# Kernel tuning notes

Hardware: AMD Instinct MI355X
Metric: run time of the kernel (lower is better)

The kernel has to match this reference:

```python
import jax, jax.numpy as jnp
import numpy as np
from jax import lax

B, SQ, SK, D, K = 4, 2048, 2048, 1024, 3


def setup_inputs() -> dict:
    key = jax.random.key(0)
    ks = jax.random.split(key, 16)
    s = 0.02
    return {
        "query_hidden": jax.random.normal(ks[0], (B, SQ, D), jnp.float32),
        "memory_hidden": jax.random.normal(ks[1], (B, SK, D), jnp.float32),
        "attention_mask": jax.random.randint(ks[2], (SQ, SK), 0, 2).astype(bool),
        # Linear projections (torch: y = x @ W.T + b)
        "q_w": jax.random.normal(ks[3], (D, D), jnp.float32) * s,
        "q_b": jnp.zeros((D,), jnp.float32),
        "k_w": jax.random.normal(ks[4], (D, D), jnp.float32) * s,
        "k_b": jnp.zeros((D,), jnp.float32),
        "v_w": jax.random.normal(ks[5], (D, D), jnp.float32) * s,
        "v_b": jnp.zeros((D,), jnp.float32),
        "o_w": jax.random.normal(ks[6], (D, D), jnp.float32) * s,
        "o_b": jnp.zeros((D,), jnp.float32),
        # ConvTransform1D: depthwise conv kernels [D,1,K], bias [D], scalar gate
        "q_kernel": jax.random.normal(ks[7], (D, 1, K), jnp.float32) * s,
        "q_cbias": jnp.zeros((D,), jnp.float32),
        "q_gate": jnp.zeros((), jnp.float32),
        "k_kernel": jax.random.normal(ks[8], (D, 1, K), jnp.float32) * s,
        "k_cbias": jnp.zeros((D,), jnp.float32),
        "k_gate": jnp.zeros((), jnp.float32),
        "v_kernel": jax.random.normal(ks[9], (D, 1, K), jnp.float32) * s,
        "v_cbias": jnp.zeros((D,), jnp.float32),
        "v_gate": jnp.zeros((), jnp.float32),
    }


def _conv_transform(x, kernel, cbias, gate):
    """Gated depthwise 1D conv along seq: x + tanh(gate) * dwconv(x). x: [B,S,D]."""
    xc = jnp.transpose(x, (0, 2, 1))  # [B,D,S]
    y = lax.conv_general_dilated(
        xc, kernel, window_strides=(1,), padding="SAME",
        dimension_numbers=("NCH", "OIH", "NCH"), feature_group_count=x.shape[-1])
    y = y + cbias[None, :, None]
    return x + jnp.tanh(gate) * jnp.transpose(y, (0, 2, 1))


def reference(query_hidden, memory_hidden, attention_mask,
              q_w, q_b, k_w, k_b, v_w, v_b, o_w, o_b,
              q_kernel, q_cbias, q_gate,
              k_kernel, k_cbias, k_gate,
              v_kernel, v_cbias, v_gate):
    d_model = query_hidden.shape[-1]
    q = _conv_transform(query_hidden @ q_w.T + q_b, q_kernel, q_cbias, q_gate)
    k = _conv_transform(memory_hidden @ k_w.T + k_b, k_kernel, k_cbias, k_gate)
    v = _conv_transform(memory_hidden @ v_w.T + v_b, v_kernel, v_cbias, v_gate)
    # [B,Sq,Sk]
    logits = jnp.einsum("bqd,bkd->bqk", q, k) / jnp.sqrt(jnp.float32(d_model))
    mask = attention_mask[None, :, :]  # broadcast like torch unsqueeze(0)
    logits = jnp.where(mask, logits, jnp.finfo(logits.dtype).min)
    attn = jax.nn.softmax(logits, axis=-1)
    out = jnp.einsum("bqk,bkd->bqd", attn, v) @ o_w.T + o_b
    return out
```

## Files before the change

### kernel.cpp

```cpp
#include <hip/hip_runtime.h>
#include <cstdint>
#include <cstddef>


#define GLOBAL_AS __attribute__((address_space(1)))
#define LDS_AS    __attribute__((address_space(3)))

typedef _Float16 h8 __attribute__((ext_vector_type(8)));
typedef float    f4_t __attribute__((ext_vector_type(4)));
typedef unsigned short us8 __attribute__((ext_vector_type(8)));

__device__ __forceinline__ float bf2f(unsigned short u) {
    union { unsigned int i; float f; } x; x.i = ((unsigned int)u) << 16; return x.f;
}
__device__ __forceinline__ float rd(const void* p, long i, int isBf) {
    return isBf ? bf2f(((const unsigned short*)p)[i]) : ((const float*)p)[i];
}

struct Probe16 { const unsigned short* p[16]; int n[16]; };

__global__ void k_probes(Probe16 a, const unsigned int* __restrict__ mask,
                         int* __restrict__ flags) {
    if (blockIdx.x < 16) {
        __shared__ int cnt;
        if (threadIdx.x == 0) cnt = 0;
        __syncthreads();
        const unsigned short* s = a.p[blockIdx.x];
        const int n = a.n[blockIdx.x];
        int bad = 0;
        for (int i = threadIdx.x; i < n; i += 256) {
            int e = (s[i] >> 7) & 0xFF;
            if (e >= 0x8F || (e > 0 && e <= 0x60)) bad++;
        }
        atomicAdd(&cnt, bad);
        __syncthreads();
        if (threadIdx.x == 0) flags[blockIdx.x] = (cnt * 4 > n) ? 0 : 1;
    } else {
        __shared__ int vi32, vf32, vbf, vf16;
        if (threadIdx.x == 0) { vi32 = vf32 = vbf = vf16 = 0; }
        __syncthreads();
        int bi32 = 0, bf32 = 0, bbf = 0, bf16c = 0;
        for (int i = threadIdx.x; i < 4096; i += 256) {
            unsigned int w = mask[i];
            if (!(w == 0u || w == 1u)) bi32++;
            if (!(w == 0u || w == 0x3F800000u)) bf32++;
            unsigned int h0 = w & 0xFFFFu, h1 = w >> 16;
            if (!((h0 == 0u || h0 == 0x3F80u) && (h1 == 0u || h1 == 0x3F80u))) bbf++;
            if (!((h0 == 0u || h0 == 0x3C00u) && (h1 == 0u || h1 == 0x3C00u))) bf16c++;
        }
        if (bi32) atomicAdd(&vi32, 1);
        if (bf32) atomicAdd(&vf32, 1);
        if (bbf)  atomicAdd(&vbf, 1);
        if (bf16c) atomicAdd(&vf16, 1);
        __syncthreads();
        if (threadIdx.x == 0) {
            int w;
            if (vi32 == 0) w = 4;
            else if (vf32 == 0) w = 4;
            else if (vbf == 0) w = 2;
            else if (vf16 == 0) w = 2;
            else w = 1;
            flags[16] = w;
        }
    }
}

__device__ __forceinline__ h8 cvt8(const void* src, size_t off8, int isBf) {
    h8 d;
    if (isBf) {
        us8 s = *(const us8*)((const unsigned short*)src + off8 * 8);
#pragma unroll
        for (int u = 0; u < 8; ++u) d[u] = (_Float16)bf2f(s[u]);
    } else {
        const float* f = (const float*)src + off8 * 8;
        f4_t a = *(const f4_t*)f;
        f4_t b = *(const f4_t*)(f + 4);
#pragma unroll
        for (int u = 0; u < 4; ++u) { d[u] = (_Float16)a[u]; d[4 + u] = (_Float16)b[u]; }
    }
    return d;
}

struct Ptr4 { const void* p[4]; };

__global__ void k_prep(const void* __restrict__ qh, const void* __restrict__ mh,
                       _Float16* __restrict__ h16dst,
                       Ptr4 wsrc, _Float16* __restrict__ w16dst,
                       const int* __restrict__ flags) {
    const int bid = blockIdx.x, tid = threadIdx.x;
    if (bid < 8192) {
        int i = bid * 256 + tid;
        int seg = i >> 20, off = i & 1048575;
        h8 d = cvt8(seg ? mh : qh, off, flags[seg]);
        *(h8*)(h16dst + (size_t)i * 8) = d;
    } else {
        int i = (bid - 8192) * 256 + tid;
        int seg = i >> 17, off = i & 131071;
        h8 d = cvt8(wsrc.p[seg], off, flags[2 + seg]);
        *(h8*)(w16dst + (size_t)i * 8) = d;
    }
}

struct ConvSrc { const void* kern[3]; const void* cb[3]; const void* gate[3]; };
__global__ void k_conv_params(ConvSrc p, const int* __restrict__ flags,
                              _Float16* __restrict__ out, float* __restrict__ tg, int D) {
#pragma unroll
    for (int t = 0; t < 3; ++t) {
        const int kIs = flags[6 + t], cIs = flags[13 + t];
        for (int d = threadIdx.x; d < D; d += 256) {
#pragma unroll
            for (int j = 0; j < 3; ++j)
                out[t * 3 * D + j * D + d] = (_Float16)rd(p.kern[t], (long)d * 3 + j, kIs);
            out[9 * D + t * D + d] = (_Float16)rd(p.cb[t], d, cIs);
        }
    }
    if (threadIdx.x < 3) {
        const void* g = p.gate[threadIdx.x];
        float gv = rd(g, 0, ((const unsigned int*)g)[0] == 0u ? 1 : 0);
        tg[threadIdx.x] = tanhf(gv);
    }
}

template <int MODE, int MTILE>
__global__ __launch_bounds__(256, 4) void k_gemm_nt(
    const _Float16* __restrict__ A, const _Float16* __restrict__ Bm,
    void* __restrict__ Cout,
    const void* __restrict__ bias, const int* __restrict__ biasFlag,
    const void* __restrict__ bias2, const int* __restrict__ biasFlag2,
    int N, int K, long sA, long sB, long sC,
    int NT, int BZ) {

    constexpr int NI = (MTILE == 128) ? 4 : 2;
    constexpr int NCA = MTILE / 32;
    __shared__ __align__(16) _Float16 As[MTILE * 64];
    __shared__ __align__(16) _Float16 Bs[128 * 64];

    const long id = blockIdx.x;
    const int xcd = (int)(id & 7);
    const long local = id >> 3;
    const int col = (int)(local % NT);
    const long g = (local / NT) * 8 + xcd;
    const int bz = (int)(g % BZ);
    const int brow = (int)(g / BZ);

    const int tid  = threadIdx.x;
    const int wave = tid >> 6, lane = tid & 63;
    const int wm = (wave >> 1) * (MTILE / 2), wn = (wave & 1) * 64;
    const int lr = lane & 15, lq = lane >> 4;

    const _Float16* Ab = A + (long)bz * sA + (size_t)brow * MTILE * K;
    const _Float16* Bb = Bm + (long)bz * sB + (size_t)col * 128 * K;

    f4_t acc[NI][4] = {};

    const _Float16* gA[NCA];
    _Float16* lA[NCA];
#pragma unroll
    for (int j = 0; j < NCA; ++j) {
        int c = tid + j * 256;
        int r = c >> 3, s = ((c & 7) - r) & 7;
        gA[j] = Ab + (size_t)r * K + s * 8;
        lA[j] = As + c * 8;
    }
    const _Float16* gB[4];
    _Float16* lB[4];
#pragma unroll
    for (int j = 0; j < 4; ++j) {
        int c = tid + j * 256;
        int r = c >> 3, s = ((c & 7) - r) & 7;
        gB[j] = Bb + (size_t)r * K + s * 8;
        lB[j] = Bs + c * 8;
    }

    for (int kb = 0; kb < K; kb += 64) {
#pragma unroll
        for (int j = 0; j < NCA; ++j)
            __builtin_amdgcn_global_load_lds((void GLOBAL_AS*)(gA[j] + kb), (void LDS_AS*)lA[j], 16, 0, 0);
#pragma unroll
        for (int j = 0; j < 4; ++j)
            __builtin_amdgcn_global_load_lds((void GLOBAL_AS*)(gB[j] + kb), (void LDS_AS*)lB[j], 16, 0, 0);
        __syncthreads();

#pragma unroll
        for (int t = 0; t < 2; ++t) {
            const int fs = ((t * 4 + lq + lr) & 7) * 8;
            h8 af[NI], bfr[4];
#pragma unroll
            for (int i = 0; i < NI; ++i) af[i]  = *(const h8*)&As[(wm + i * 16 + lr) * 64 + fs];
#pragma unroll
            for (int j = 0; j < 4; ++j) bfr[j] = *(const h8*)&Bs[(wn + j * 16 + lr) * 64 + fs];
#pragma unroll
            for (int i = 0; i < NI; ++i)
#pragma unroll
                for (int j = 0; j < 4; ++j)
                    acc[i][j] = __builtin_amdgcn_mfma_f32_16x16x32_f16(af[i], bfr[j], acc[i][j], 0, 0, 0);
        }
        __syncthreads();
    }

    const long row0 = (long)brow * MTILE + wm + lq * 4;
    const long col0 = (long)col * 128 + wn + lr;

    float bv[4];
    if constexpr (MODE != 0) {
        const void* bp = bias; const int* bfp = biasFlag; long boff = 0;
        if (bias2 != nullptr && col * 128 >= (N >> 1)) {
            bp = bias2; bfp = biasFlag2; boff = (long)(N >> 1);
        }
        const int bIs = *bfp;
#pragma unroll
        for (int j = 0; j < 4; ++j) bv[j] = rd(bp, col0 + j * 16 - boff, bIs);
    } else {
#pragma unroll
        for (int j = 0; j < 4; ++j) bv[j] = 0.0f;
    }
    if constexpr (MODE == 2) {
        float* C = (float*)Cout + (long)bz * sC;
#pragma unroll
        for (int i = 0; i < NI; ++i)
#pragma unroll
            for (int j = 0; j < 4; ++j)
#pragma unroll
                for (int r = 0; r < 4; ++r)
                    C[(row0 + i * 16 + r) * (long)N + col0 + j * 16] = acc[i][j][r] + bv[j];
    } else {
        _Float16* C = (_Float16*)Cout + (long)bz * sC;
#pragma unroll
        for (int i = 0; i < NI; ++i)
#pragma unroll
            for (int j = 0; j < 4; ++j)
#pragma unroll
                for (int r = 0; r < 4; ++r) {
                    float v = acc[i][j][r] + bv[j];
                    v = fminf(fmaxf(v, -65000.0f), 65000.0f);
                    C[(row0 + i * 16 + r) * (long)N + col0 + j * 16] = (_Float16)v;
                }
    }
}

template <int MODE>
__global__ __launch_bounds__(512, 2) void k_gemm16(
    const _Float16* __restrict__ A, const _Float16* __restrict__ Bm,
    void* __restrict__ Cout,
    const void* __restrict__ bias, const int* __restrict__ biasFlag,
    const void* __restrict__ bias2, const int* __restrict__ biasFlag2,
    int N, int K, long sA, long sB, long sC,
    float scale, const void* __restrict__ mraw, const int* __restrict__ mwf,
    int NT, int BZ) {

    __shared__ __align__(16) _Float16 AS[2][2][8192];
    __shared__ __align__(16) _Float16 BS[2][2][8192];

    const long id = blockIdx.x;
    const int xcd = (int)(id & 7);
    const long local = id >> 3;
    const int col = (int)(local % NT);
    const long g = (local / NT) * 8 + xcd;
    const int bz = (int)(g % BZ);
    const int brow = (int)(g / BZ);

    const int tid  = threadIdx.x;
    const int wave = tid >> 6, lane = tid & 63;
    const int wr = wave >> 2, wc = wave & 3;
    const int lr = lane & 15, lq = lane >> 4;

    const _Float16* Ab = A + (long)bz * sA + (size_t)brow * 256 * K;
    const _Float16* Bb = Bm + (long)bz * sB + (size_t)col * 256 * K;

    f4_t acc[8][4] = {};

    const _Float16* gAsrc[2][2];
    const _Float16* gBsrc[2][2];
    int lOff[2];
#pragma unroll
    for (int j = 0; j < 2; ++j) {
        int c = tid + j * 512;
        int rho = c >> 3, s = ((c & 7) - rho) & 7;
        lOff[j] = c * 8;
#pragma unroll
        for (int gg = 0; gg < 2; ++gg) {
            int ra = gg * 64 + (rho & 63) + (rho >> 6) * 128;
            gAsrc[gg][j] = Ab + (size_t)ra * K + s * 8;
            int rb = gg * 32 + (rho & 31) + (rho >> 5) * 64;
            gBsrc[gg][j] = Bb + (size_t)rb * K + s * 8;
        }
    }

#define STAGE_A(buf, gg, kb)                                                              \
    do {                                                                                  \
        __builtin_amdgcn_global_load_lds((void GLOBAL_AS*)(gAsrc[gg][0] + (kb)),          \
                                         (void LDS_AS*)&AS[buf][gg][lOff[0]], 16, 0, 0);  \
        __builtin_amdgcn_global_load_lds((void GLOBAL_AS*)(gAsrc[gg][1] + (kb)),          \
                                         (void LDS_AS*)&AS[buf][gg][lOff[1]], 16, 0, 0);  \
    } while (0)
#define STAGE_B(buf, gg, kb)                                                              \
    do {                                                                                  \
        __builtin_amdgcn_global_load_lds((void GLOBAL_AS*)(gBsrc[gg][0] + (kb)),          \
                                         (void LDS_AS*)&BS[buf][gg][lOff[0]], 16, 0, 0);  \
        __builtin_amdgcn_global_load_lds((void GLOBAL_AS*)(gBsrc[gg][1] + (kb)),          \
                                         (void LDS_AS*)&BS[buf][gg][lOff[1]], 16, 0, 0);  \
    } while (0)

    const int nkt = K >> 6;

    STAGE_A(0, 0, 0);
    STAGE_B(0, 0, 0);
    STAGE_B(0, 1, 0);
    STAGE_A(0, 1, 0);
    asm volatile("s_waitcnt vmcnt(4)" ::: "memory");
    __builtin_amdgcn_s_barrier();

    int cur = 0;
    for (int t = 0; t < nkt; ++t) {
        const bool pf = (t + 1) < nkt;
        const long kb = (long)(t + 1) << 6;
        const int nx = cur ^ 1;
        h8 a0[4][2], a1[4][2], b0[2][2], b1[2][2];

#pragma unroll
        for (int ks = 0; ks < 2; ++ks) {
#pragma unroll
            for (int m = 0; m < 4; ++m) {
                int rho = wr * 64 + m * 16 + lr;
                a0[m][ks] = *(const h8*)&AS[cur][0][rho * 64 + ((ks * 4 + lq + rho) & 7) * 8];
            }
#pragma unroll
            for (int n = 0; n < 2; ++n) {
                int rho = wc * 32 + n * 16 + lr;
                b0[n][ks] = *(const h8*)&BS[cur][0][rho * 64 + ((ks * 4 + lq + rho) & 7) * 8];
            }
        }
        if (pf) STAGE_A(nx, 0, kb);
        __builtin_amdgcn_s_barrier();
        __builtin_amdgcn_s_setprio(1);
#pragma unroll
        for (int ks = 0; ks < 2; ++ks)
#pragma unroll
            for (int m = 0; m < 4; ++m)
#pragma unroll
                for (int n = 0; n < 2; ++n)
                    acc[m][n] = __builtin_amdgcn_mfma_f32_16x16x32_f16(
                        a0[m][ks], b0[n][ks], acc[m][n], 0, 0, 0);
        __builtin_amdgcn_s_setprio(0);
        if (pf) asm volatile("s_waitcnt vmcnt(4)" ::: "memory");
        else    asm volatile("s_waitcnt vmcnt(2)" ::: "memory");
        __builtin_amdgcn_s_barrier();

#pragma unroll
        for (int ks = 0; ks < 2; ++ks)
#pragma unroll
            for (int n = 0; n < 2; ++n) {
                int rho = wc * 32 + n * 16 + lr;
                b1[n][ks] = *(const h8*)&BS[cur][1][rho * 64 + ((ks * 4 + lq + rho) & 7) * 8];
            }
        if (pf) STAGE_B(nx, 0, kb);
        __builtin_amdgcn_s_barrier();
        __builtin_amdgcn_s_setprio(1);
#pragma unroll
        for (int ks = 0; ks < 2; ++ks)
#pragma unroll
            for (int m = 0; m < 4; ++m)
#pragma unroll
                for (int n = 0; n < 2; ++n)
                    acc[m][2 + n] = __builtin_amdgcn_mfma_f32_16x16x32_f16(
                        a0[m][ks], b1[n][ks], acc[m][2 + n], 0, 0, 0);
        __builtin_amdgcn_s_setprio(0);
        if (pf) asm volatile("s_waitcnt vmcnt(4)" ::: "memory");
        else    asm volatile("s_waitcnt vmcnt(0)" ::: "memory");
        __builtin_amdgcn_s_barrier();

#pragma unroll
        for (int ks = 0; ks < 2; ++ks)
#pragma unroll
            for (int m = 0; m < 4; ++m) {
                int rho = wr * 64 + m * 16 + lr;
                a1[m][ks] = *(const h8*)&AS[cur][1][rho * 64 + ((ks * 4 + lq + rho) & 7) * 8];
            }
        if (pf) STAGE_B(nx, 1, kb);
        __builtin_amdgcn_s_barrier();
        __builtin_amdgcn_s_setprio(1);
#pragma unroll
        for (int ks = 0; ks < 2; ++ks)
#pragma unroll
            for (int m = 0; m < 4; ++m)
#pragma unroll
                for (int n = 0; n < 2; ++n)
                    acc[4 + m][2 + n] = __builtin_amdgcn_mfma_f32_16x16x32_f16(
                        a1[m][ks], b1[n][ks], acc[4 + m][2 + n], 0, 0, 0);
        __builtin_amdgcn_s_setprio(0);
        __builtin_amdgcn_s_barrier();

#pragma unroll
        for (int ks = 0; ks < 2; ++ks)
#pragma unroll
            for (int n = 0; n < 2; ++n) {
                int rho = wc * 32 + n * 16 + lr;
                b0[n][ks] = *(const h8*)&BS[cur][0][rho * 64 + ((ks * 4 + lq + rho) & 7) * 8];
            }
        if (pf) STAGE_A(nx, 1, kb);
        __builtin_amdgcn_s_barrier();
        __builtin_amdgcn_s_setprio(1);
#pragma unroll
        for (int ks = 0; ks < 2; ++ks)
#pragma unroll
            for (int m = 0; m < 4; ++m)
#pragma unroll
                for (int n = 0; n < 2; ++n)
                    acc[4 + m][n] = __builtin_amdgcn_mfma_f32_16x16x32_f16(
                        a1[m][ks], b0[n][ks], acc[4 + m][n], 0, 0, 0);
        __builtin_amdgcn_s_setprio(0);
        if (pf) asm volatile("s_waitcnt vmcnt(4)" ::: "memory");
        __builtin_amdgcn_s_barrier();
        cur = nx;
    }
#undef STAGE_A
#undef STAGE_B

    const long row0 = (long)brow * 256 + wr * 128 + lq * 4;
    const long col0 = (long)col * 256 + wc * 64 + lr;

    if constexpr (MODE == 3) {
        const int mw = *mwf;
        _Float16* C = (_Float16*)Cout + (long)bz * sC;
#pragma unroll
        for (int i = 0; i < 8; ++i)
#pragma unroll
            for (int j = 0; j < 4; ++j)
#pragma unroll
                for (int r = 0; r < 4; ++r) {
                    long row = row0 + i * 16 + r;
                    long ccol = col0 + j * 16;
                    long mi = row * (long)N + ccol;
                    bool keep;
                    if (mw == 4)      keep = ((const unsigned int*)mraw)[mi] != 0u;
                    else if (mw == 2) keep = ((const unsigned short*)mraw)[mi] != 0;
                    else              keep = ((const unsigned char*)mraw)[mi] != 0;
                    float v = acc[i][j][r] * scale;
                    v = fminf(fmaxf(v, -60000.0f), 60000.0f);
                    C[row * (long)N + ccol] = (_Float16)(keep ? v : -60000.0f);
                }
    } else {
        float bv[4];
        {
            const void* bp = bias; const int* bfp = biasFlag; long boff = 0;
            if (bias2 != nullptr && col * 256 >= (N >> 1)) {
                bp = bias2; bfp = biasFlag2; boff = (long)(N >> 1);
            }
            const int bIs = *bfp;
#pragma unroll
            for (int j = 0; j < 4; ++j) bv[j] = rd(bp, col0 + j * 16 - boff, bIs);
        }
        _Float16* C = (_Float16*)Cout + (long)bz * sC;
#pragma unroll
        for (int i = 0; i < 8; ++i)
#pragma unroll
            for (int j = 0; j < 4; ++j)
#pragma unroll
                for (int r = 0; r < 4; ++r) {
                    float v = acc[i][j][r] + bv[j];
                    v = fminf(fmaxf(v, -65000.0f), 65000.0f);
                    C[(row0 + i * 16 + r) * (long)N + col0 + j * 16] = (_Float16)v;
                }
    }
}

struct ConvP {
    const _Float16* x; int xs; _Float16* y;
    const _Float16* kp; const _Float16* cb; const float* tg;
};
__global__ void k_convs(ConvP p0, ConvP p1,
                        const _Float16* __restrict__ xv, int xvs,
                        _Float16* __restrict__ vt,
                        const _Float16* __restrict__ kpv,
                        const _Float16* __restrict__ cbv,
                        const float* __restrict__ tgv,
                        int S, int SK, int D) {
    __shared__ _Float16 T[64][65];
    const int bid = blockIdx.x, tid = threadIdx.x;
    h8 zero;
#pragma unroll
    for (int u = 0; u < 8; ++u) zero[u] = (_Float16)0.0f;

    if (bid < 8192) {
        const ConvP& p = (bid >= 4096) ? p1 : p0;
        int l = bid & 4095;
        int b = l >> 10, sp = l & 1023;
        int s = sp * 2 + (tid >> 7);
        int d0 = (tid & 127) * 8;
        const size_t xb = ((size_t)b * S + s) * p.xs + d0;
        const size_t yb = ((size_t)b * S + s) * D + d0;
        h8 xc = *(const h8*)(p.x + xb);
        h8 xp = (s > 0)     ? *(const h8*)(p.x + xb - p.xs) : zero;
        h8 xn = (s < S - 1) ? *(const h8*)(p.x + xb + p.xs) : zero;
        h8 k0 = *(const h8*)(p.kp + 0 * D + d0);
        h8 k1 = *(const h8*)(p.kp + 1 * D + d0);
        h8 k2 = *(const h8*)(p.kp + 2 * D + d0);
        h8 cb = *(const h8*)(p.cb + d0);
        float tg = *p.tg;
        h8 o;
#pragma unroll
        for (int u = 0; u < 8; ++u) {
            float cv = (float)xp[u] * (float)k0[u] + (float)xc[u] * (float)k1[u] +
                       (float)xn[u] * (float)k2[u] + (float)cb[u];
            float v = (float)xc[u] + tg * cv;
            o[u] = (_Float16)fminf(fmaxf(v, -65000.0f), 65000.0f);
        }
        *(h8*)(p.y + yb) = o;
    } else {
        int l = bid - 8192;
        int bx = l & 31, by = (l >> 5) & 15, b = l >> 9;
        int s0 = bx * 64, d0 = by * 64;
        float tg = *tgv;
#pragma unroll
        for (int it = 0; it < 2; ++it) {
            int idx = it * 256 + tid;
            int r = idx >> 3, c = (idx & 7) * 8;
            int s = s0 + r;
            const size_t xb = ((size_t)b * SK + s) * xvs + d0 + c;
            h8 xc = *(const h8*)(xv + xb);
            h8 xp = (s > 0)      ? *(const h8*)(xv + xb - xvs) : zero;
            h8 xn = (s < SK - 1) ? *(const h8*)(xv + xb + xvs) : zero;
            h8 k0 = *(const h8*)(kpv + 0 * D + d0 + c);
            h8 k1 = *(const h8*)(kpv + 1 * D + d0 + c);
            h8 k2 = *(const h8*)(kpv + 2 * D + d0 + c);
            h8 cb = *(const h8*)(cbv + d0 + c);
#pragma unroll
            for (int u = 0; u < 8; ++u) {
                float cv = (float)xp[u] * (float)k0[u] + (float)xc[u] * (float)k1[u] +
                           (float)xn[u] * (float)k2[u] + (float)cb[u];
                float v = (float)xc[u] + tg * cv;
                T[r][c + u] = (_Float16)fminf(fmaxf(v, -65000.0f), 65000.0f);
            }
        }
        __syncthreads();
#pragma unroll
        for (int it = 0; it < 2; ++it) {
            int idx = it * 256 + tid;
            int dr = idx >> 3, c = (idx & 7) * 8;
            h8 o;
#pragma unroll
            for (int u = 0; u < 8; ++u) o[u] = T[c + u][dr];
            *(h8*)(vt + ((size_t)b * D + d0 + dr) * SK + s0 + c) = o;
        }
    }
}

__global__ __launch_bounds__(256) void k_softmax(const _Float16* __restrict__ sc,
                                                 _Float16* __restrict__ pr, int SK) {
    const long row = blockIdx.x;
    const int tid = threadIdx.x, lane = tid & 63, wave = tid >> 6;
    h8 v = *(const h8*)(sc + row * (long)SK + tid * 8);
    float f[8]; float mx = -3.0e38f;
#pragma unroll
    for (int u = 0; u < 8; ++u) { f[u] = (float)v[u]; mx = fmaxf(mx, f[u]); }
#pragma unroll
    for (int o = 32; o > 0; o >>= 1) mx = fmaxf(mx, __shfl_xor(mx, o, 64));
    __shared__ float red[8];
    if (lane == 0) red[wave] = mx;
    __syncthreads();
    mx = fmaxf(fmaxf(red[0], red[1]), fmaxf(red[2], red[3]));
    float sum = 0.0f;
#pragma unroll
    for (int u = 0; u < 8; ++u) { f[u] = __expf(f[u] - mx); sum += f[u]; }
#pragma unroll
    for (int o = 32; o > 0; o >>= 1) sum += __shfl_xor(sum, o, 64);
    if (lane == 0) red[4 + wave] = sum;
    __syncthreads();
    sum = red[4] + red[5] + red[6] + red[7];
    float inv = 1.0f / sum;
    h8 o8;
#pragma unroll
    for (int u = 0; u < 8; ++u) o8[u] = (_Float16)(f[u] * inv);
    *(h8*)(pr + row * (long)SK + tid * 8) = o8;
}

extern "C" void kernel_launch(void* const* d_in, const int* in_sizes, int n_in,
                              void* d_out, int out_size, void* d_ws, size_t ws_size,
                              hipStream_t stream) {
    const int Bn = 4, SQ = 2048, SK = 2048, D = 1024;
    const size_t nQ = (size_t)Bn * SQ * D;

    const void* qh = d_in[0];
    const void* mh = d_in[1];
    const void* mask = d_in[2];
    const void* q_w = d_in[3];
    const void* q_b = d_in[4];
    const void* k_w = d_in[5];
    const void* k_b = d_in[6];
    const void* v_w = d_in[7];
    const void* v_b = d_in[8];
    const void* o_w = d_in[9];
    const void* o_b = d_in[10];
    const void* q_kern = d_in[11];
    const void* q_cb   = d_in[12];
    const void* q_g    = d_in[13];
    const void* k_kern = d_in[14];
    const void* k_cb   = d_in[15];
    const void* k_g    = d_in[16];
    const void* v_kern = d_in[17];
    const void* v_cb   = d_in[18];
    const void* v_g    = d_in[19];

    char* ws = (char*)d_ws;
    _Float16* scores   = (_Float16*)(ws + 0);
    _Float16* attn_out = (_Float16*)(ws + 0);
    _Float16* w16      = (_Float16*)(ws + 33554432);
    _Float16* par16    = (_Float16*)(ws + 37748736);
    float*    tgf      = (float*)(ws + 37748736 + 12 * 1024 * 2);
    _Float16* lin      = (_Float16*)(ws + 41943040);
    _Float16* lin_q    = lin;
    _Float16* lin_kv   = lin + nQ;
    _Float16* probs    = lin;
    _Float16* conv     = (_Float16*)(ws + 92274688);
    _Float16* qh16     = conv;
    _Float16* mh16     = conv + nQ;
    _Float16* vt       = (_Float16*)(ws + 125829120);
    int*      flags    = (int*)(ws + 142606336);

    Probe16 pa;
    const void* pp[16] = {qh, mh, q_w, k_w, v_w, o_w, q_kern, k_kern, v_kern,
                          q_b, k_b, v_b, o_b, q_cb, k_cb, v_cb};
    const int   pn[16] = {2048, 2048, 2048, 2048, 2048, 2048, 3072, 3072, 3072,
                          1024, 1024, 1024, 1024, 1024, 1024, 1024};
    for (int i = 0; i < 16; ++i) { pa.p[i] = (const unsigned short*)pp[i]; pa.n[i] = pn[i]; }
    k_probes<<<17, 256, 0, stream>>>(pa, (const unsigned int*)mask, flags);

    Ptr4 wp; wp.p[0] = q_w; wp.p[1] = k_w; wp.p[2] = v_w; wp.p[3] = o_w;
    k_prep<<<10240, 256, 0, stream>>>(qh, mh, qh16, wp, w16, flags);

    k_gemm_nt<1, 64><<<dim3(1024), 256, 0, stream>>>(
        qh16, w16, lin_q, q_b, flags + 9, nullptr, nullptr,
        D, D, 0, 0, 0, 8, 1);
    k_gemm16<1><<<dim3(256), 512, 0, stream>>>(
        mh16, w16 + (size_t)D * D, lin_kv, k_b, flags + 10, v_b, flags + 11,
        2 * D, D, 0, 0, 0, 1.0f, nullptr, nullptr, 8, 1);

    ConvSrc cs;
    cs.kern[0] = q_kern; cs.kern[1] = k_kern; cs.kern[2] = v_kern;
    cs.cb[0] = q_cb; cs.cb[1] = k_cb; cs.cb[2] = v_cb;
    cs.gate[0] = q_g; cs.gate[1] = k_g; cs.gate[2] = v_g;
    k_conv_params<<<1, 256, 0, stream>>>(cs, flags, par16, tgf, D);

    ConvP cq{lin_q, D, conv + 0 * nQ, par16 + 0 * 3 * D, par16 + 9 * D + 0 * D, tgf + 0};
    ConvP ck{lin_kv, 2 * D, conv + 1 * nQ, par16 + 1 * 3 * D, par16 + 9 * D + 1 * D, tgf + 1};
    k_convs<<<dim3(10240), 256, 0, stream>>>(
        cq, ck, lin_kv + D, 2 * D, vt, par16 + 2 * 3 * D, par16 + 9 * D + 2 * D, tgf + 2,
        SQ, SK, D);

    k_gemm16<3><<<dim3(256), 512, 0, stream>>>(
        conv + 0 * nQ, conv + 1 * nQ, scores, nullptr, nullptr, nullptr, nullptr,
        SK, D, (long)SQ * D, (long)SK * D, (long)SQ * SK, 0.03125f, mask, flags + 16, 8, 4);

    k_softmax<<<Bn * SQ, 256, 0, stream>>>(scores, probs, SK);

    k_gemm_nt<0, 64><<<dim3(1024), 256, 0, stream>>>(
        probs, vt, attn_out, nullptr, nullptr, nullptr, nullptr,
        D, SK, (long)SQ * SK, (long)D * SK, (long)SQ * D, 8, 4);

    k_gemm_nt<2, 64><<<dim3(1024), 256, 0, stream>>>(
        attn_out, w16 + 3 * (size_t)D * D, d_out, o_b, flags + 12, nullptr, nullptr,
        D, D, 0, 0, 0, 8, 1);

    (void)in_sizes; (void)n_in; (void)out_size; (void)ws_size;
}
```

Baseline: 444.9 us.

## Move attention mask application from QK GEMM epilogue into softmax; fold conv params into prep

The mask lookup moves out of the QK^T GEMM epilogue and into the softmax kernel. The GEMM epilogue no longer does scattered per-element mask loads, and softmax reads the mask row with vector loads alongside the scores. The separate single-block conv-parameter kernel is merged into k_prep as one extra block, which saves a launch. The par16/tgf workspace region is relocated, and the extra block performs the small parameter conversion serially.

```diff
diff --git a/kernel.cpp b/kernel.cpp
--- a/kernel.cpp
+++ b/kernel.cpp
@@ -82,10 +82,13 @@
 }
 
 struct Ptr4 { const void* p[4]; };
+struct ConvSrc { const void* kern[3]; const void* cb[3]; const void* gate[3]; };
 
 __global__ void k_prep(const void* __restrict__ qh, const void* __restrict__ mh,
                        _Float16* __restrict__ h16dst,
                        Ptr4 wsrc, _Float16* __restrict__ w16dst,
+                       ConvSrc cs, _Float16* __restrict__ par16,
+                       float* __restrict__ tgf,
                        const int* __restrict__ flags) {
     const int bid = blockIdx.x, tid = threadIdx.x;
     if (bid < 8192) {
@@ -93,31 +96,28 @@
         int seg = i >> 20, off = i & 1048575;
         h8 d = cvt8(seg ? mh : qh, off, flags[seg]);
         *(h8*)(h16dst + (size_t)i * 8) = d;
-    } else {
+    } else if (bid < 10240) {
         int i = (bid - 8192) * 256 + tid;
         int seg = i >> 17, off = i & 131071;
         h8 d = cvt8(wsrc.p[seg], off, flags[2 + seg]);
         *(h8*)(w16dst + (size_t)i * 8) = d;
-    }
-}
-
-struct ConvSrc { const void* kern[3]; const void* cb[3]; const void* gate[3]; };
-__global__ void k_conv_params(ConvSrc p, const int* __restrict__ flags,
-                              _Float16* __restrict__ out, float* __restrict__ tg, int D) {
-#pragma unroll
-    for (int t = 0; t < 3; ++t) {
-        const int kIs = flags[6 + t], cIs = flags[13 + t];
-        for (int d = threadIdx.x; d < D; d += 256) {
-#pragma unroll
-            for (int j = 0; j < 3; ++j)
-                out[t * 3 * D + j * D + d] = (_Float16)rd(p.kern[t], (long)d * 3 + j, kIs);
-            out[9 * D + t * D + d] = (_Float16)rd(p.cb[t], d, cIs);
-        }
-    }
-    if (threadIdx.x < 3) {
-        const void* g = p.gate[threadIdx.x];
-        float gv = rd(g, 0, ((const unsigned int*)g)[0] == 0u ? 1 : 0);
-        tg[threadIdx.x] = tanhf(gv);
+    } else {
+        const int D = 1024;
+#pragma unroll
+        for (int t = 0; t < 3; ++t) {
+            const int kIs = flags[6 + t], cIs = flags[13 + t];
+            for (int d = tid; d < D; d += 256) {
+#pragma unroll
+                for (int j = 0; j < 3; ++j)
+                    par16[t * 3 * D + j * D + d] = (_Float16)rd(cs.kern[t], (long)d * 3 + j, kIs);
+                par16[9 * D + t * D + d] = (_Float16)rd(cs.cb[t], d, cIs);
+            }
+        }
+        if (tid < 3) {
+            const void* g = cs.gate[tid];
+            float gv = rd(g, 0, ((const unsigned int*)g)[0] == 0u ? 1 : 0);
+            tgf[tid] = tanhf(gv);
+        }
     }
 }
 
@@ -245,8 +245,7 @@
     const void* __restrict__ bias, const int* __restrict__ biasFlag,
     const void* __restrict__ bias2, const int* __restrict__ biasFlag2,
     int N, int K, long sA, long sB, long sC,
-    float scale, const void* __restrict__ mraw, const int* __restrict__ mwf,
-    int NT, int BZ) {
+    float scale, int NT, int BZ) {
 
     __shared__ __align__(16) _Float16 AS[2][2][8192];
     __shared__ __align__(16) _Float16 BS[2][2][8192];
@@ -420,7 +419,6 @@
     const long col0 = (long)col * 256 + wc * 64 + lr;
 
     if constexpr (MODE == 3) {
-        const int mw = *mwf;
         _Float16* C = (_Float16*)Cout + (long)bz * sC;
 #pragma unroll
         for (int i = 0; i < 8; ++i)
@@ -428,16 +426,9 @@
             for (int j = 0; j < 4; ++j)
 #pragma unroll
                 for (int r = 0; r < 4; ++r) {
-                    long row = row0 + i * 16 + r;
-                    long ccol = col0 + j * 16;
-                    long mi = row * (long)N + ccol;
-                    bool keep;
-                    if (mw == 4)      keep = ((const unsigned int*)mraw)[mi] != 0u;
-                    else if (mw == 2) keep = ((const unsigned short*)mraw)[mi] != 0;
-                    else              keep = ((const unsigned char*)mraw)[mi] != 0;
                     float v = acc[i][j][r] * scale;
                     v = fminf(fmaxf(v, -60000.0f), 60000.0f);
-                    C[row * (long)N + ccol] = (_Float16)(keep ? v : -60000.0f);
+                    C[(row0 + i * 16 + r) * (long)N + col0 + j * 16] = (_Float16)v;
                 }
     } else {
         float bv[4];
@@ -546,13 +537,37 @@
 }
 
 __global__ __launch_bounds__(256) void k_softmax(const _Float16* __restrict__ sc,
-                                                 _Float16* __restrict__ pr, int SK) {
+                                                 _Float16* __restrict__ pr,
+                                                 const void* __restrict__ mraw,
+                                                 const int* __restrict__ mwf,
+                                                 int SK) {
     const long row = blockIdx.x;
     const int tid = threadIdx.x, lane = tid & 63, wave = tid >> 6;
     h8 v = *(const h8*)(sc + row * (long)SK + tid * 8);
+
+    const int mw = *mwf;
+    const long mbase = (row & 2047) * (long)SK + tid * 8;
+    unsigned int km = 0;
+    if (mw == 4) {
+        const unsigned int* mp = (const unsigned int*)mraw + mbase;
+#pragma unroll
+        for (int u = 0; u < 8; ++u) km |= (mp[u] != 0u) ? (1u << u) : 0u;
+    } else if (mw == 2) {
+        const us8 m8 = *(const us8*)((const unsigned short*)mraw + mbase);
+#pragma unroll
+        for (int u = 0; u < 8; ++u) km |= (m8[u] != 0) ? (1u << u) : 0u;
+    } else {
+        unsigned long long m8 = *(const unsigned long long*)((const unsigned char*)mraw + mbase);
+#pragma unroll
+        for (int u = 0; u < 8; ++u) km |= ((m8 >> (8 * u)) & 0xFFull) ? (1u << u) : 0u;
+    }
+
     float f[8]; float mx = -3.0e38f;
 #pragma unroll
-    for (int u = 0; u < 8; ++u) { f[u] = (float)v[u]; mx = fmaxf(mx, f[u]); }
+    for (int u = 0; u < 8; ++u) {
+        f[u] = (km & (1u << u)) ? (float)v[u] : -60000.0f;
+        mx = fmaxf(mx, f[u]);
+    }
 #pragma unroll
     for (int o = 32; o > 0; o >>= 1) mx = fmaxf(mx, __shfl_xor(mx, o, 64));
     __shared__ float red[8];
@@ -604,9 +619,9 @@
     char* ws = (char*)d_ws;
     _Float16* scores   = (_Float16*)(ws + 0);
     _Float16* attn_out = (_Float16*)(ws + 0);
+    _Float16* par16    = (_Float16*)(ws + 33521664);
+    float*    tgf      = (float*)(ws + 33521664 + 24576);
     _Float16* w16      = (_Float16*)(ws + 33554432);
-    _Float16* par16    = (_Float16*)(ws + 37748736);
-    float*    tgf      = (float*)(ws + 37748736 + 12 * 1024 * 2);
     _Float16* lin      = (_Float16*)(ws + 41943040);
     _Float16* lin_q    = lin;
     _Float16* lin_kv   = lin + nQ;
@@ -626,20 +641,18 @@
     k_probes<<<17, 256, 0, stream>>>(pa, (const unsigned int*)mask, flags);
 
     Ptr4 wp; wp.p[0] = q_w; wp.p[1] = k_w; wp.p[2] = v_w; wp.p[3] = o_w;
-    k_prep<<<10240, 256, 0, stream>>>(qh, mh, qh16, wp, w16, flags);
+    ConvSrc cs;
+    cs.kern[0] = q_kern; cs.kern[1] = k_kern; cs.kern[2] = v_kern;
+    cs.cb[0] = q_cb; cs.cb[1] = k_cb; cs.cb[2] = v_cb;
+    cs.gate[0] = q_g; cs.gate[1] = k_g; cs.gate[2] = v_g;
+    k_prep<<<10241, 256, 0, stream>>>(qh, mh, qh16, wp, w16, cs, par16, tgf, flags);
 
     k_gemm_nt<1, 64><<<dim3(1024), 256, 0, stream>>>(
         qh16, w16, lin_q, q_b, flags + 9, nullptr, nullptr,
         D, D, 0, 0, 0, 8, 1);
     k_gemm16<1><<<dim3(256), 512, 0, stream>>>(
         mh16, w16 + (size_t)D * D, lin_kv, k_b, flags + 10, v_b, flags + 11,
-        2 * D, D, 0, 0, 0, 1.0f, nullptr, nullptr, 8, 1);
-
-    ConvSrc cs;
-    cs.kern[0] = q_kern; cs.kern[1] = k_kern; cs.kern[2] = v_kern;
-    cs.cb[0] = q_cb; cs.cb[1] = k_cb; cs.cb[2] = v_cb;
-    cs.gate[0] = q_g; cs.gate[1] = k_g; cs.gate[2] = v_g;
-    k_conv_params<<<1, 256, 0, stream>>>(cs, flags, par16, tgf, D);
+        2 * D, D, 0, 0, 0, 1.0f, 8, 1);
 
     ConvP cq{lin_q, D, conv + 0 * nQ, par16 + 0 * 3 * D, par16 + 9 * D + 0 * D, tgf + 0};
     ConvP ck{lin_kv, 2 * D, conv + 1 * nQ, par16 + 1 * 3 * D, par16 + 9 * D + 1 * D, tgf + 1};
@@ -649,9 +662,9 @@
 
     k_gemm16<3><<<dim3(256), 512, 0, stream>>>(
         conv + 0 * nQ, conv + 1 * nQ, scores, nullptr, nullptr, nullptr, nullptr,
-        SK, D, (long)SQ * D, (long)SK * D, (long)SQ * SK, 0.03125f, mask, flags + 16, 8, 4);
-
-    k_softmax<<<Bn * SQ, 256, 0, stream>>>(scores, probs, SK);
+        SK, D, (long)SQ * D, (long)SK * D, (long)SQ * SK, 0.03125f, 8, 4);
+
+    k_softmax<<<Bn * SQ, 256, 0, stream>>>(scores, probs, mask, flags + 16, SK);
 
     k_gemm_nt<0, 64><<<dim3(1024), 256, 0, stream>>>(
         probs, vt, attn_out, nullptr, nullptr, nullptr, nullptr,
```

Measured after the change: 393.8 us. 1.13x faster.
